# Kernel tuning notes

Hardware: AMD Instinct MI355X
Metric: run time of the kernel (lower is better)

The kernel has to match this reference:

```python
import jax, jax.numpy as jnp
import numpy as np

N_NODES = 50000
N_EDGES = 800000
C_IN = 128
C_OUT = 128


def setup_inputs() -> dict:
    key = jax.random.key(0)
    k1, k2, k3 = jax.random.split(key, 3)
    x = jax.random.normal(k1, (N_NODES, C_IN), dtype=jnp.float32)
    edge_index = jax.random.randint(k2, (2, N_EDGES), 0, N_NODES, dtype=jnp.int64)
    # Glorot-style init for the GCN weight, zero bias (PyG defaults)
    scale = jnp.sqrt(2.0 / (C_IN + C_OUT)).astype(jnp.float32)
    weight = jax.random.normal(k3, (C_IN, C_OUT), dtype=jnp.float32) * scale
    bias = jnp.zeros((C_OUT,), dtype=jnp.float32)
    return {"x": x, "edge_index": edge_index, "weight": weight, "bias": bias}


def reference(x, edge_index, weight, bias):
    # GCNConv (edge_weight=None): out = D^-1/2 (A+I) D^-1/2 (x @ W) + b, then ReLU.
    # Dropout is identity in eval mode.
    n = x.shape[0]
    loops = jnp.arange(n, dtype=edge_index.dtype)
    src = jnp.concatenate([edge_index[0], loops])  # [E+N] message sources j
    dst = jnp.concatenate([edge_index[1], loops])  # [E+N] aggregation targets i
    ew = jnp.ones(src.shape[0], dtype=x.dtype)
    # degree computed at target nodes (PyG gcn_norm uses col)
    deg = jax.ops.segment_sum(ew, dst, num_segments=n)
    deg_inv_sqrt = jnp.where(deg > 0, jax.lax.rsqrt(jnp.maximum(deg, 1.0)), 0.0)
    norm = deg_inv_sqrt[src] * deg_inv_sqrt[dst]  # [E+N]
    h = x @ weight                                 # [N, C_out]
    msg = h[src] * norm[:, None]                   # gather + scale  [E+N, C_out]
    agg = jax.ops.segment_sum(msg, dst, num_segments=n)  # scatter-add SpMM
    return jax.nn.relu(agg + bias)
```

## Files before the change

kernel.cpp:

```cpp
#include <hip/hip_runtime.h>
#include <cstdint>
#include <cstddef>

#define NCH 128
#define GEMM_ROWS 64
#define XPAD 136
#define CAP 64

typedef short bf16x8 __attribute__((ext_vector_type(8)));
typedef float f32x4 __attribute__((ext_vector_type(4)));

__device__ __forceinline__ int detect_is64(const unsigned int* __restrict__ ei) {
  unsigned int v = ei[((threadIdx.x & 63) << 1) + 1];
  return (__ballot(v != 0u) == 0ULL) ? 1 : 0;
}

__device__ __forceinline__ unsigned short f2bf(float x) {
  unsigned int u = __float_as_uint(x);
  u += 0x7fffu + ((u >> 16) & 1u);
  return (unsigned short)(u >> 16);
}

__device__ __forceinline__ int ei_at(const void* ei, long long i, int is64) {
  return is64 ? (int)((const long long*)ei)[i] : ((const int*)ei)[i];
}

__global__ __launch_bounds__(256) void k_gemm_fill(
    const float* __restrict__ x, const float* __restrict__ W,
    unsigned short* __restrict__ g, int N, const void* __restrict__ ei, int E,
    int* __restrict__ cnt, unsigned short* __restrict__ bucket, int gbl) {
  if ((int)blockIdx.x >= gbl) {
    int is64 = detect_is64((const unsigned int*)ei);
    int base = ((int)blockIdx.x - gbl) * 2048 + (int)threadIdx.x * 8;
    if (base >= E) return;
    if (base + 8 <= E) {
      int s[8], d[8];
      if (is64) {
        const long long* ps = (const long long*)ei + base;
        const long long* pd = (const long long*)ei + E + base;
#pragma unroll
        for (int j = 0; j < 8; ++j) { s[j] = (int)ps[j]; d[j] = (int)pd[j]; }
      } else {
        const int4* ps = (const int4*)((const int*)ei + base);
        const int4* pd = (const int4*)((const int*)ei + E + base);
        int4 a = ps[0], b = ps[1], c = pd[0], dd = pd[1];
        s[0] = a.x; s[1] = a.y; s[2] = a.z; s[3] = a.w;
        s[4] = b.x; s[5] = b.y; s[6] = b.z; s[7] = b.w;
        d[0] = c.x; d[1] = c.y; d[2] = c.z; d[3] = c.w;
        d[4] = dd.x; d[5] = dd.y; d[6] = dd.z; d[7] = dd.w;
      }
      int slot[8];
#pragma unroll
      for (int j = 0; j < 8; ++j) slot[j] = atomicAdd(&cnt[d[j]], 1);
#pragma unroll
      for (int j = 0; j < 8; ++j)
        if (slot[j] < CAP)
          bucket[(size_t)d[j] * CAP + slot[j]] = (unsigned short)s[j];
    } else {
      for (int j = 0; j < 8; ++j)
        if (base + j < E) {
          int s = ei_at(ei, base + j, is64);
          int d = ei_at(ei, (long long)E + base + j, is64);
          int slot = atomicAdd(&cnt[d], 1);
          if (slot < CAP) bucket[(size_t)d * CAP + slot] = (unsigned short)s;
        }
    }
    return;
  }
  __shared__ unsigned short xbf[GEMM_ROWS * XPAD];
  int t = threadIdx.x;
  int row0 = (int)blockIdx.x * GEMM_ROWS;
#pragma unroll
  for (int j = 0; j < 8; ++j) {
    int idx = t + 256 * j;
    int r = idx >> 5, ch = idx & 31;
    int row = row0 + r;
    float4 v = (row < N) ? ((const float4*)(x + (size_t)row * NCH))[ch]
                         : make_float4(0.f, 0.f, 0.f, 0.f);
    ushort4 p;
    p.x = f2bf(v.x); p.y = f2bf(v.y); p.z = f2bf(v.z); p.w = f2bf(v.w);
    *(ushort4*)&xbf[r * XPAD + ch * 4] = p;
  }
  int lane = t & 63, wv = t >> 6;
  int n0 = wv * 32, l15 = lane & 15, q = lane >> 4;
  bf16x8 B[4][2];
#pragma unroll
  for (int ks = 0; ks < 4; ++ks)
#pragma unroll
    for (int nt = 0; nt < 2; ++nt) {
      int n = n0 + nt * 16 + l15;
      bf16x8 b;
#pragma unroll
      for (int j = 0; j < 8; ++j)
        b[j] = (short)f2bf(W[(size_t)(ks * 32 + q * 8 + j) * NCH + n]);
      B[ks][nt] = b;
    }
  __syncthreads();
  f32x4 acc[4][2];
#pragma unroll
  for (int mt = 0; mt < 4; ++mt)
#pragma unroll
    for (int nt = 0; nt < 2; ++nt)
#pragma unroll
      for (int i = 0; i < 4; ++i) acc[mt][nt][i] = 0.f;
#pragma unroll
  for (int ks = 0; ks < 4; ++ks) {
#pragma unroll
    for (int mt = 0; mt < 4; ++mt) {
      bf16x8 a = *(const bf16x8*)&xbf[(mt * 16 + l15) * XPAD + ks * 32 + q * 8];
      acc[mt][0] = __builtin_amdgcn_mfma_f32_16x16x32_bf16(a, B[ks][0], acc[mt][0], 0, 0, 0);
      acc[mt][1] = __builtin_amdgcn_mfma_f32_16x16x32_bf16(a, B[ks][1], acc[mt][1], 0, 0, 0);
    }
  }
#pragma unroll
  for (int mt = 0; mt < 4; ++mt) {
#pragma unroll
    for (int reg = 0; reg < 4; ++reg) {
      int rl = mt * 16 + q * 4 + reg;
      int row = row0 + rl;
      if (row < N) {
        size_t base = (size_t)row * NCH + n0;
        g[base + l15]      = f2bf(acc[mt][0][reg]);
        g[base + 16 + l15] = f2bf(acc[mt][1][reg]);
      }
    }
  }
}

__device__ __forceinline__ void acc8(float* a, uint4 v, float w) {
  a[0] = fmaf(__uint_as_float(v.x << 16), w, a[0]);
  a[1] = fmaf(__uint_as_float(v.x & 0xffff0000u), w, a[1]);
  a[2] = fmaf(__uint_as_float(v.y << 16), w, a[2]);
  a[3] = fmaf(__uint_as_float(v.y & 0xffff0000u), w, a[3]);
  a[4] = fmaf(__uint_as_float(v.z << 16), w, a[4]);
  a[5] = fmaf(__uint_as_float(v.z & 0xffff0000u), w, a[5]);
  a[6] = fmaf(__uint_as_float(v.w << 16), w, a[6]);
  a[7] = fmaf(__uint_as_float(v.w & 0xffff0000u), w, a[7]);
}

__global__ __launch_bounds__(256) void k_agg(const unsigned short* __restrict__ g,
                                             const int* __restrict__ cnt,
                                             const unsigned short* __restrict__ bucket,
                                             const float* __restrict__ bias,
                                             float* __restrict__ out, int N) {
  int i = blockIdx.x * 4 + (threadIdx.x >> 6);
  if (i >= N) return;
  int lane = threadIdx.x & 63;
  int grp = lane >> 4, sl = lane & 15;
  float a[8];
#pragma unroll
  for (int k = 0; k < 8; ++k) a[k] = 0.f;
  int deg = cnt[i];
  float di = rsqrtf((float)(deg + 1));
  int m = deg < CAP ? deg : CAP;
  if (grp == 0) {
    uint4 v = *(const uint4*)(g + (size_t)i * NCH + sl * 8);
    acc8(a, v, di);
  }
  const unsigned short* brow = bucket + (size_t)i * CAP;
  int e = 0;
  for (; e + 16 <= m; e += 16) {
    ushort4 sv = *(const ushort4*)(brow + e + 4 * grp);
    int s[4] = {sv.x, sv.y, sv.z, sv.w};
    uint4 v[4];
    float w[4];
#pragma unroll
    for (int j = 0; j < 4; ++j) {
      v[j] = *(const uint4*)(g + (size_t)s[j] * NCH + sl * 8);
      w[j] = rsqrtf((float)(cnt[s[j]] + 1));
    }
#pragma unroll
    for (int j = 0; j < 4; ++j) acc8(a, v[j], w[j]);
  }
  for (; e < m; e += 4) {
    int idx = e + grp;
    int cl = idx < m ? idx : m - 1;
    int s = brow[cl];
    float w = (idx < m) ? rsqrtf((float)(cnt[s] + 1)) : 0.f;
    uint4 v = *(const uint4*)(g + (size_t)s * NCH + sl * 8);
    acc8(a, v, w);
  }
#pragma unroll
  for (int k = 0; k < 8; ++k) {
    a[k] += __shfl_xor(a[k], 16);
    a[k] += __shfl_xor(a[k], 32);
  }
  if (grp == 0) {
    const float4* bb = (const float4*)bias;
    float4 b0 = bb[sl * 2], b1 = bb[sl * 2 + 1];
    f32x4 o0, o1;
    o0[0] = fmaxf(fmaf(a[0], di, b0.x), 0.f);
    o0[1] = fmaxf(fmaf(a[1], di, b0.y), 0.f);
    o0[2] = fmaxf(fmaf(a[2], di, b0.z), 0.f);
    o0[3] = fmaxf(fmaf(a[3], di, b0.w), 0.f);
    o1[0] = fmaxf(fmaf(a[4], di, b1.x), 0.f);
    o1[1] = fmaxf(fmaf(a[5], di, b1.y), 0.f);
    o1[2] = fmaxf(fmaf(a[6], di, b1.z), 0.f);
    o1[3] = fmaxf(fmaf(a[7], di, b1.w), 0.f);
    float* op = out + (size_t)i * NCH + sl * 8;
    __builtin_nontemporal_store(o0, (f32x4*)op);
    __builtin_nontemporal_store(o1, (f32x4*)(op + 4));
  }
}

extern "C" void kernel_launch(void* const* d_in, const int* in_sizes, int n_in,
                              void* d_out, int out_size, void* d_ws, size_t ws_size,
                              hipStream_t stream) {
  const float* x    = (const float*)d_in[0];
  const void*  ei   = d_in[1];
  const float* W    = (const float*)d_in[2];
  const float* bias = (const float*)d_in[3];
  float* out = (float*)d_out;

  int N = out_size / NCH;
  int E = in_sizes[1] / 2;

  char* ws = (char*)d_ws;
  size_t off = 0;
  auto alloc = [&](size_t bytes) -> char* {
    char* p = ws + off;
    off = (off + bytes + 255) & ~(size_t)255;
    return p;
  };
  char* zbase = ws;
  int*            cnt    = (int*)alloc((size_t)N * 4);
  size_t zbytes = off;
  unsigned short* bucket = (unsigned short*)alloc((size_t)N * CAP * 2);
  unsigned short* g      = (unsigned short*)alloc((size_t)N * NCH * 2);
  (void)ws_size;

  int gbl  = (N + GEMM_ROWS - 1) / GEMM_ROWS;
  int cbl8 = (E + 2047) / 2048;

  (void)hipMemsetAsync(zbase, 0, zbytes, stream);
  k_gemm_fill<<<gbl + cbl8, 256, 0, stream>>>(x, W, g, N, ei, E, cnt, bucket, gbl);
  k_agg<<<(N + 3) / 4, 256, 0, stream>>>(g, cnt, bucket, bias, out, N);
}
```

Measured before the change: 159.8 us.

## Replace global-atomic bucket fill with two-pass partitioned binning through LDS histograms

Edge bucketing is split into two passes. First, edges are partitioned by the high bits of the destination into 256-node partitions, using an LDS histogram and one global atomic per partition per block. Then a new k_bin kernel bins each partition into per-node buckets with LDS atomics and writes the degree counts. This removes 800K scattered global atomics on cnt, at the cost of an extra kernel launch, an intermediate pbuf round trip, and a fixed per-partition capacity (PCAP) that can overflow.

```diff
diff --git a/kernel.cpp b/kernel.cpp
--- a/kernel.cpp
+++ b/kernel.cpp
@@ -6,6 +6,8 @@
 #define GEMM_ROWS 64
 #define XPAD 136
 #define CAP 64
+#define PCAP 5120
+#define SMEM_BYTES 17408
 
 typedef short bf16x8 __attribute__((ext_vector_type(8)));
 typedef float f32x4 __attribute__((ext_vector_type(4)));
@@ -25,16 +27,23 @@
   return is64 ? (int)((const long long*)ei)[i] : ((const int*)ei)[i];
 }
 
-__global__ __launch_bounds__(256) void k_gemm_fill(
+__global__ __launch_bounds__(256) void k_gemm_part(
     const float* __restrict__ x, const float* __restrict__ W,
     unsigned short* __restrict__ g, int N, const void* __restrict__ ei, int E,
-    int* __restrict__ cnt, unsigned short* __restrict__ bucket, int gbl) {
+    int* __restrict__ pcount, unsigned int* __restrict__ pbuf, int gbl) {
+  __shared__ char smem[SMEM_BYTES];
+  int t = threadIdx.x;
   if ((int)blockIdx.x >= gbl) {
+    int* hist  = (int*)smem;
+    int* gbase = (int*)smem + 256;
     int is64 = detect_is64((const unsigned int*)ei);
-    int base = ((int)blockIdx.x - gbl) * 2048 + (int)threadIdx.x * 8;
-    if (base >= E) return;
+    hist[t] = 0;
+    __syncthreads();
+    int base = ((int)blockIdx.x - gbl) * 2048 + t * 8;
+    int s[8], d[8], ord[8], p[8];
+    int nv = 0;
     if (base + 8 <= E) {
-      int s[8], d[8];
+      nv = 8;
       if (is64) {
         const long long* ps = (const long long*)ei + base;
         const long long* pd = (const long long*)ei + E + base;
@@ -49,26 +58,34 @@
         d[0] = c.x; d[1] = c.y; d[2] = c.z; d[3] = c.w;
         d[4] = dd.x; d[5] = dd.y; d[6] = dd.z; d[7] = dd.w;
       }
-      int slot[8];
-#pragma unroll
-      for (int j = 0; j < 8; ++j) slot[j] = atomicAdd(&cnt[d[j]], 1);
-#pragma unroll
-      for (int j = 0; j < 8; ++j)
-        if (slot[j] < CAP)
-          bucket[(size_t)d[j] * CAP + slot[j]] = (unsigned short)s[j];
-    } else {
-      for (int j = 0; j < 8; ++j)
-        if (base + j < E) {
-          int s = ei_at(ei, base + j, is64);
-          int d = ei_at(ei, (long long)E + base + j, is64);
-          int slot = atomicAdd(&cnt[d], 1);
-          if (slot < CAP) bucket[(size_t)d * CAP + slot] = (unsigned short)s;
-        }
-    }
+    } else if (base < E) {
+      nv = E - base;
+      for (int j = 0; j < nv; ++j) {
+        s[j] = ei_at(ei, base + j, is64);
+        d[j] = ei_at(ei, (long long)E + base + j, is64);
+      }
+    }
+#pragma unroll
+    for (int j = 0; j < 8; ++j)
+      if (j < nv) {
+        p[j] = d[j] >> 8;
+        ord[j] = atomicAdd(&hist[p[j]], 1);
+      }
+    __syncthreads();
+    int h = hist[t];
+    gbase[t] = (h > 0) ? atomicAdd(&pcount[t], h) : 0;
+    __syncthreads();
+#pragma unroll
+    for (int j = 0; j < 8; ++j)
+      if (j < nv) {
+        int slot = gbase[p[j]] + ord[j];
+        if (slot < PCAP)
+          pbuf[(size_t)p[j] * PCAP + slot] =
+              (unsigned int)s[j] | ((unsigned int)(d[j] & 255) << 16);
+      }
     return;
   }
-  __shared__ unsigned short xbf[GEMM_ROWS * XPAD];
-  int t = threadIdx.x;
+  unsigned short* xbf = (unsigned short*)smem;
   int row0 = (int)blockIdx.x * GEMM_ROWS;
 #pragma unroll
   for (int j = 0; j < 8; ++j) {
@@ -125,6 +142,30 @@
       }
     }
   }
+}
+
+__global__ __launch_bounds__(256) void k_bin(const unsigned int* __restrict__ pbuf,
+                                             const int* __restrict__ pcount,
+                                             unsigned short* __restrict__ bucket,
+                                             int* __restrict__ cnt, int N) {
+  __shared__ int cnt2[256];
+  int p = blockIdx.x, t = threadIdx.x;
+  cnt2[t] = 0;
+  __syncthreads();
+  int count = pcount[p];
+  if (count > PCAP) count = PCAP;
+  const unsigned int* buf = pbuf + (size_t)p * PCAP;
+  for (int k = t; k < count; k += 256) {
+    unsigned int rec = buf[k];
+    int low = (rec >> 16) & 255;
+    int s = rec & 0xFFFF;
+    int ord = atomicAdd(&cnt2[low], 1);
+    if (ord < CAP)
+      bucket[((size_t)((p << 8) + low)) * CAP + ord] = (unsigned short)s;
+  }
+  __syncthreads();
+  int i = (p << 8) + t;
+  if (i < N) cnt[i] = cnt2[t];
 }
 
 __device__ __forceinline__ void acc8(float* a, uint4 v, float w) {
@@ -214,6 +255,7 @@
 
   int N = out_size / NCH;
   int E = in_sizes[1] / 2;
+  int NP = (N + 255) >> 8;
 
   char* ws = (char*)d_ws;
   size_t off = 0;
@@ -223,9 +265,11 @@
     return p;
   };
   char* zbase = ws;
-  int*            cnt    = (int*)alloc((size_t)N * 4);
+  int*            pcount = (int*)alloc((size_t)256 * 4);
   size_t zbytes = off;
+  unsigned int*   pbuf   = (unsigned int*)alloc((size_t)NP * PCAP * 4);
   unsigned short* bucket = (unsigned short*)alloc((size_t)N * CAP * 2);
+  int*            cnt    = (int*)alloc((size_t)NP * 256 * 4);
   unsigned short* g      = (unsigned short*)alloc((size_t)N * NCH * 2);
   (void)ws_size;
 
@@ -233,6 +277,7 @@
   int cbl8 = (E + 2047) / 2048;
 
   (void)hipMemsetAsync(zbase, 0, zbytes, stream);
-  k_gemm_fill<<<gbl + cbl8, 256, 0, stream>>>(x, W, g, N, ei, E, cnt, bucket, gbl);
+  k_gemm_part<<<gbl + cbl8, 256, 0, stream>>>(x, W, g, N, ei, E, pcount, pbuf, gbl);
+  k_bin<<<NP, 256, 0, stream>>>(pbuf, pcount, bucket, cnt, N);
   k_agg<<<(N + 3) / 4, 256, 0, stream>>>(g, cnt, bucket, bias, out, N);
 }
```

Result: faster. 142.0 us (-11.1%).
